# Optimization experiments

Measured on AMD Instinct MI355X. Metric: run time of the kernel, lower is better.

## Reference

```python
import jax, jax.numpy as jnp
import numpy as np

IOU_THRESHOLD = 0.5
LOW_BG_IOU = 0.1      # below this -> ignored
IMG_SIZE = 1024.0


def _make_boxes(key, n):
    kxy, kwh = jax.random.split(key)
    xy = jax.random.uniform(kxy, (n, 2), dtype=jnp.float32, maxval=IMG_SIZE * 0.8)
    wh = jax.random.uniform(kwh, (n, 2), dtype=jnp.float32, minval=8.0, maxval=IMG_SIZE * 0.2)
    return jnp.concatenate([xy, xy + wh], axis=-1)  # valid x1<x2, y1<y2


def setup_inputs() -> dict:
    key = jax.random.key(0)
    k1, k2, k3 = jax.random.split(key, 3)
    proposals = _make_boxes(k1, 200000)          # [N,4]
    gt_boxes = _make_boxes(k2, 128)              # [G,4]
    gt_labels = jax.random.randint(k3, (128,), 1, 21, dtype=jnp.int64)  # [G]
    return {"proposals": proposals, "gt_boxes": gt_boxes, "gt_labels": gt_labels}


def get_iou(boxes1, boxes2):
    # boxes1: [G,4], boxes2: [N,4] -> iou [G,N]
    area1 = (boxes1[:, 2] - boxes1[:, 0]) * (boxes1[:, 3] - boxes1[:, 1])  # [G]
    area2 = (boxes2[:, 2] - boxes2[:, 0]) * (boxes2[:, 3] - boxes2[:, 1])  # [N]
    x1 = jnp.maximum(boxes1[:, None, 0], boxes2[None, :, 0])
    y1 = jnp.maximum(boxes1[:, None, 1], boxes2[None, :, 1])
    x2 = jnp.minimum(boxes1[:, None, 2], boxes2[None, :, 2])
    y2 = jnp.minimum(boxes1[:, None, 3], boxes2[None, :, 3])
    inter = jnp.clip(x2 - x1, 0.0) * jnp.clip(y2 - y1, 0.0)  # [G,N]
    union = area1[:, None] + area2[None, :] - inter
    return inter / union


def reference(proposals, gt_boxes, gt_labels):
    iou = get_iou(gt_boxes, proposals)                # [G,N]
    best_match_iou = jnp.max(iou, axis=0)             # [N]
    best_match_gt_idx = jnp.argmax(iou, axis=0)       # [N], >= 0
    background = (best_match_iou < IOU_THRESHOLD) & (best_match_iou >= LOW_BG_IOU)
    ignored = best_match_iou < LOW_BG_IOU
    # torch clamps the (-1/-2) sentinel indices back to 0 before the gather,
    # so gathering with the raw argmax index is identical.
    matched_gt_boxes = gt_boxes[best_match_gt_idx]    # [N,4]
    labels = gt_labels[best_match_gt_idx].astype(jnp.int64)
    labels = jnp.where(background, jnp.int64(0), labels)
    labels = jnp.where(ignored, jnp.int64(-1), labels)
    return labels, matched_gt_boxes
```

## Files before the change

### kernel.cpp

```cpp
#include <hip/hip_runtime.h>


#define BLOCK 256
#define NPROP 64
#define GT_TOTAL 128
#define GT_PER_WAVE 32
#define IOU_THRESHOLD 0.5f
#define LOW_BG_IOU 0.1f

__global__ __launch_bounds__(BLOCK) void roi_match_kernel(
    const float* __restrict__ proposals,
    const float* __restrict__ gt_boxes,
    const int*   __restrict__ gt_labels,
    float* __restrict__ out,
    int N)
{
#pragma clang fp contract(off)
    __shared__ float  s_rec[GT_TOTAL][8];
    __shared__ float4 s_part[4][NPROP];

    int tid = threadIdx.x;
    if (tid < GT_TOTAL) {
        float4 b = ((const float4*)gt_boxes)[tid];
        s_rec[tid][0] = b.x; s_rec[tid][1] = b.y;
        s_rec[tid][2] = b.z; s_rec[tid][3] = b.w;
        s_rec[tid][4] = (b.z - b.x) * (b.w - b.y);
        s_rec[tid][5] = (float)gt_labels[tid];
        s_rec[tid][6] = 0.0f; s_rec[tid][7] = 0.0f;
    }
    __syncthreads();

    int wave = tid >> 6;
    int lane = tid & 63;
    int n  = blockIdx.x * NPROP + lane;
    int nc = n < N ? n : N - 1;

    float4 p = ((const float4*)proposals)[nc];
    float area_p = (p.z - p.x) * (p.w - p.y);

    int g0 = wave * GT_PER_WAVE;
    int   bi = g0;
    float inter_b = 0.0f, uni_b = 1.0f;

#pragma unroll 4
    for (int j = 0; j < GT_PER_WAVE; ++j) {
        int g = g0 + j;
        float4 gb   = *(const float4*)&s_rec[g][0];
        float garea = s_rec[g][4];

        float x1 = fmaxf(gb.x, p.x);
        float y1 = fmaxf(gb.y, p.y);
        float x2 = fminf(gb.z, p.z);
        float y2 = fminf(gb.w, p.w);
        float iw = fmaxf(x2 - x1, 0.0f);
        float ih = fmaxf(y2 - y1, 0.0f);
        float inter = iw * ih;
        float uni   = (garea + area_p) - inter;

        float p1 = inter * uni_b;
        float e1 = fmaf(inter, uni_b, -p1);
        float p2 = inter_b * uni;
        float e2 = fmaf(inter_b, uni, -p2);
        bool gt = (p1 - p2) > (e2 - e1);

        bi      = gt ? g     : bi;
        inter_b = gt ? inter : inter_b;
        uni_b   = gt ? uni   : uni_b;
    }

    s_part[wave][lane] = make_float4(inter_b, uni_b, __int_as_float(bi), 0.0f);
    __syncthreads();

    if (wave == 0 && n < N) {
        float4 b0 = s_part[0][lane];
        float binter = b0.x, buni = b0.y;
        int   bbi = __float_as_int(b0.z);
#pragma unroll
        for (int w = 1; w < 4; ++w) {
            float4 c = s_part[w][lane];
            float ci = c.x, cu = c.y;
            float p1 = ci * buni;
            float e1 = fmaf(ci, buni, -p1);
            float p2 = binter * cu;
            float e2 = fmaf(binter, cu, -p2);
            bool gt = (p1 - p2) > (e2 - e1);
            bbi    = gt ? __float_as_int(c.z) : bbi;
            binter = gt ? ci : binter;
            buni   = gt ? cu : buni;
        }

        float best = binter / buni;

        float lab;
        if (best < LOW_BG_IOU)          lab = -1.0f;
        else if (best < IOU_THRESHOLD)  lab = 0.0f;
        else                            lab = s_rec[bbi][5];

        out[n] = lab;
        ((float4*)(out + N))[n] = *(const float4*)&s_rec[bbi][0];
    }
}

extern "C" void kernel_launch(void* const* d_in, const int* in_sizes, int n_in,
                              void* d_out, int out_size, void* d_ws, size_t ws_size,
                              hipStream_t stream) {
    const float* proposals = (const float*)d_in[0];
    const float* gt_boxes  = (const float*)d_in[1];
    const int*   gt_labels = (const int*)d_in[2];
    float* out = (float*)d_out;

    int N = in_sizes[0] / 4;
    int blocks = (N + NPROP - 1) / NPROP;

    roi_match_kernel<<<blocks, BLOCK, 0, stream>>>(proposals, gt_boxes,
                                                   gt_labels, out, N);
}
```

Measured before the change: 72.50 us.

## Precompute GT records in a prep kernel and read them via scalar loads

```diff
diff --git a/kernel.cpp b/kernel.cpp
--- a/kernel.cpp
+++ b/kernel.cpp
@@ -8,29 +8,35 @@
 #define IOU_THRESHOLD 0.5f
 #define LOW_BG_IOU 0.1f
 
+typedef __attribute__((ext_vector_type(8))) float float8;
+
+__global__ __launch_bounds__(GT_TOTAL) void prep_kernel(
+    const float* __restrict__ gt_boxes,
+    const int*   __restrict__ gt_labels,
+    float*       __restrict__ rec)
+{
+#pragma clang fp contract(off)
+    int g = threadIdx.x;
+    float4 b = ((const float4*)gt_boxes)[g];
+    float8 r;
+    r[0] = b.x; r[1] = b.y; r[2] = b.z; r[3] = b.w;
+    r[4] = (b.z - b.x) * (b.w - b.y);
+    r[5] = (float)gt_labels[g];
+    r[6] = 0.0f; r[7] = 0.0f;
+    ((float8*)rec)[g] = r;
+}
+
 __global__ __launch_bounds__(BLOCK) void roi_match_kernel(
     const float* __restrict__ proposals,
-    const float* __restrict__ gt_boxes,
-    const int*   __restrict__ gt_labels,
+    const float* __restrict__ rec,
     float* __restrict__ out,
     int N)
 {
 #pragma clang fp contract(off)
-    __shared__ float  s_rec[GT_TOTAL][8];
     __shared__ float4 s_part[4][NPROP];
 
-    int tid = threadIdx.x;
-    if (tid < GT_TOTAL) {
-        float4 b = ((const float4*)gt_boxes)[tid];
-        s_rec[tid][0] = b.x; s_rec[tid][1] = b.y;
-        s_rec[tid][2] = b.z; s_rec[tid][3] = b.w;
-        s_rec[tid][4] = (b.z - b.x) * (b.w - b.y);
-        s_rec[tid][5] = (float)gt_labels[tid];
-        s_rec[tid][6] = 0.0f; s_rec[tid][7] = 0.0f;
-    }
-    __syncthreads();
-
-    int wave = tid >> 6;
+    int tid  = threadIdx.x;
+    int wave = __builtin_amdgcn_readfirstlane(tid >> 6);
     int lane = tid & 63;
     int n  = blockIdx.x * NPROP + lane;
     int nc = n < N ? n : N - 1;
@@ -45,17 +51,16 @@
 #pragma unroll 4
     for (int j = 0; j < GT_PER_WAVE; ++j) {
         int g = g0 + j;
-        float4 gb   = *(const float4*)&s_rec[g][0];
-        float garea = s_rec[g][4];
+        float8 r = ((const float8*)rec)[g];
 
-        float x1 = fmaxf(gb.x, p.x);
-        float y1 = fmaxf(gb.y, p.y);
-        float x2 = fminf(gb.z, p.z);
-        float y2 = fminf(gb.w, p.w);
+        float x1 = fmaxf(r[0], p.x);
+        float y1 = fmaxf(r[1], p.y);
+        float x2 = fminf(r[2], p.z);
+        float y2 = fminf(r[3], p.w);
         float iw = fmaxf(x2 - x1, 0.0f);
         float ih = fmaxf(y2 - y1, 0.0f);
         float inter = iw * ih;
-        float uni   = (garea + area_p) - inter;
+        float uni   = (area_p + r[4]) - inter;
 
         float p1 = inter * uni_b;
         float e1 = fmaf(inter, uni_b, -p1);
@@ -91,13 +96,16 @@
 
         float best = binter / buni;
 
+        float4 box = ((const float4*)rec)[bbi * 2];
+        float glab = rec[bbi * 8 + 5];
+
         float lab;
         if (best < LOW_BG_IOU)          lab = -1.0f;
         else if (best < IOU_THRESHOLD)  lab = 0.0f;
-        else                            lab = s_rec[bbi][5];
+        else                            lab = glab;
 
         out[n] = lab;
-        ((float4*)(out + N))[n] = *(const float4*)&s_rec[bbi][0];
+        ((float4*)(out + N))[n] = box;
     }
 }
 
@@ -108,10 +116,11 @@
     const float* gt_boxes  = (const float*)d_in[1];
     const int*   gt_labels = (const int*)d_in[2];
     float* out = (float*)d_out;
+    float* rec = (float*)d_ws;
 
     int N = in_sizes[0] / 4;
     int blocks = (N + NPROP - 1) / NPROP;
 
-    roi_match_kernel<<<blocks, BLOCK, 0, stream>>>(proposals, gt_boxes,
-                                                   gt_labels, out, N);
+    prep_kernel<<<1, GT_TOTAL, 0, stream>>>(gt_boxes, gt_labels, rec);
+    roi_match_kernel<<<blocks, BLOCK, 0, stream>>>(proposals, rec, out, N);
 }
```

Result: no change. 73.51 us (+1.4%).
